# Kernel tuning notes

Hardware: AMD Instinct MI355X
Metric: run time of the kernel (lower is better)

## Reference

```python
import jax, jax.numpy as jnp
import numpy as np

B, N, F = 4, 1024, 128
HID, EMB = 64, 32  # node_transform hidden, node embedding dim


def setup_inputs() -> dict:
    key = jax.random.key(0)
    ks = jax.random.split(key, 12)
    s = lambda fan_in: 1.0 / np.sqrt(fan_in)
    x = jax.random.normal(ks[0], (B, N, F), dtype=jnp.float32)
    adj_matrix = jax.random.uniform(ks[1], (N, N), dtype=jnp.float32)
    # node_transform: Linear(F, 64) -> ReLU -> Linear(64, 32)
    W1 = jax.random.uniform(ks[2], (F, HID), minval=-s(F), maxval=s(F))
    b1 = jax.random.uniform(ks[3], (HID,), minval=-s(F), maxval=s(F))
    W2 = jax.random.uniform(ks[4], (HID, EMB), minval=-s(HID), maxval=s(HID))
    b2 = jax.random.uniform(ks[5], (EMB,), minval=-s(HID), maxval=s(HID))
    # edge_attention: Linear(64, 32) -> ReLU -> Linear(32, 1) -> Sigmoid
    Wa1 = jax.random.uniform(ks[6], (2 * EMB, 32), minval=-s(2 * EMB), maxval=s(2 * EMB))
    ba1 = jax.random.uniform(ks[7], (32,), minval=-s(2 * EMB), maxval=s(2 * EMB))
    Wa2 = jax.random.uniform(ks[8], (32, 1), minval=-s(32), maxval=s(32))
    ba2 = jax.random.uniform(ks[9], (1,), minval=-s(32), maxval=s(32))
    return {"x": x, "adj_matrix": adj_matrix, "W1": W1, "b1": b1, "W2": W2,
            "b2": b2, "Wa1": Wa1, "ba1": ba1, "Wa2": Wa2, "ba2": ba2}


def reference(x, adj_matrix, W1, b1, W2, b2, Wa1, ba1, Wa2, ba2):
    # node_transform: [B,N,F] -> [B,N,32]
    h = jax.nn.relu(x @ W1 + b1)
    e = h @ W2 + b2  # node embeddings [B,N,EMB]
    # edge attention on concat(e_i, e_j): the first Linear on the concat
    # decomposes exactly as e_i @ Wa1[:EMB] + e_j @ Wa1[EMB:] + ba1,
    # avoiding the [B,N,N,2*EMB] concat tensor.
    a_i = e @ Wa1[:EMB]   # [B,N,32]
    a_j = e @ Wa1[EMB:]   # [B,N,32]
    pre = jax.nn.relu(a_i[:, :, None, :] + a_j[:, None, :, :] + ba1)  # [B,N,N,32]
    att = jax.nn.sigmoid(jnp.squeeze(pre @ Wa2, -1) + ba2[0])  # [B,N,N]
    att = att * adj_matrix[None, :, :]
    attended = jnp.einsum('bij,bjd->bid', att, e)  # [B,N,EMB]
    return jnp.mean(attended, axis=1)  # [B,EMB]
```

## Files before the change

kernel.cpp:

```cpp
#include <hip/hip_runtime.h>

#define B   4
#define N   1024
#define F   128
#define HID 64
#define EMB 32
#define NIC 32
#define IC  (N/NIC)
#define JB  256

__global__ __launch_bounds__(256) void k1_embed(
    const float* __restrict__ x,  const float* __restrict__ W1, const float* __restrict__ b1,
    const float* __restrict__ W2, const float* __restrict__ b2,
    const float* __restrict__ Wa1,
    float* __restrict__ e, float* __restrict__ ai, float* __restrict__ aj)
{
    __shared__ float sh_x[4][F];
    __shared__ float sh_h[4][HID];
    __shared__ float sh_e[4][EMB];
    const int tid  = threadIdx.x;
    const int w    = tid >> 6;
    const int lane = tid & 63;
    const int r    = blockIdx.x * 4 + w;

    sh_x[w][lane]      = x[(size_t)r * F + lane];
    sh_x[w][lane + 64] = x[(size_t)r * F + 64 + lane];
    __syncthreads();

    float acc = b1[lane];
    #pragma unroll 8
    for (int k = 0; k < F; ++k)
        acc = fmaf(sh_x[w][k], W1[k * HID + lane], acc);
    sh_h[w][lane] = fmaxf(acc, 0.f);
    __syncthreads();

    const int d = lane & 31;
    float ev = b2[d];
    #pragma unroll 8
    for (int k = 0; k < HID; ++k)
        ev = fmaf(sh_h[w][k], W2[k * EMB + d], ev);
    if (lane < EMB) {
        sh_e[w][d] = ev;
        e[(size_t)r * EMB + d] = ev;
    }
    __syncthreads();

    const float* Wp = Wa1 + (lane < 32 ? 0 : EMB * EMB);
    float av = 0.f;
    #pragma unroll 8
    for (int k = 0; k < EMB; ++k)
        av = fmaf(sh_e[w][k], Wp[k * EMB + d], av);
    if (lane < 32) ai[(size_t)r * EMB + d] = av;
    else           aj[(size_t)r * EMB + d] = av;
}

__global__ __launch_bounds__(256) void k2_att(
    const float* __restrict__ ai, const float* __restrict__ aj,
    const float* __restrict__ ba1, const float* __restrict__ Wa2,
    const float* __restrict__ ba2, const float* __restrict__ adj,
    float* __restrict__ s_part)
{
    const int ic   = blockIdx.x;
    const int b    = blockIdx.y >> 2;
    const int jblk = blockIdx.y & 3;
    const int tid  = threadIdx.x;
    const int j    = jblk * JB + tid;

    __shared__ float4 sh_ai[IC][EMB / 4];
    {
        const int row = tid >> 3, c4 = tid & 7;
        const float4* src = (const float4*)(ai + ((size_t)b * N + ic * IC + row) * EMB);
        sh_ai[row][c4] = src[c4];
    }

    float ajb[EMB];
    {
        const float* ap = aj + ((size_t)b * N + j) * EMB;
        #pragma unroll
        for (int d2 = 0; d2 < EMB; ++d2) ajb[d2] = ap[d2] + ba1[d2];
    }
    float w2r[EMB];
    #pragma unroll
    for (int d2 = 0; d2 < EMB; ++d2) w2r[d2] = Wa2[d2];
    const float bb = ba2[0];
    __syncthreads();

    float ssum = 0.f;
    const float* adjp = adj + (size_t)(ic * IC) * N + j;
    for (int i = 0; i < IC; ++i) {
        const float4* arow = sh_ai[i];
        float dot = bb;
        #pragma unroll
        for (int q = 0; q < EMB / 4; ++q) {
            const float4 a4 = arow[q];
            dot = fmaf(fmaxf(a4.x + ajb[4 * q + 0], 0.f), w2r[4 * q + 0], dot);
            dot = fmaf(fmaxf(a4.y + ajb[4 * q + 1], 0.f), w2r[4 * q + 1], dot);
            dot = fmaf(fmaxf(a4.z + ajb[4 * q + 2], 0.f), w2r[4 * q + 2], dot);
            dot = fmaf(fmaxf(a4.w + ajb[4 * q + 3], 0.f), w2r[4 * q + 3], dot);
        }
        const float sg = 1.f / (1.f + __expf(-dot));
        ssum = fmaf(sg, adjp[(size_t)i * N], ssum);
    }
    s_part[((size_t)b * NIC + ic) * N + j] = ssum;
}

__global__ __launch_bounds__(256) void k3_out(
    const float* __restrict__ s_part, const float* __restrict__ e,
    float* __restrict__ out)
{
    const int b   = blockIdx.x;
    const int tid = threadIdx.x;
    float acc[EMB];
    #pragma unroll
    for (int d = 0; d < EMB; ++d) acc[d] = 0.f;

    for (int j = tid; j < N; j += 256) {
        float ssum = 0.f;
        #pragma unroll 8
        for (int ic = 0; ic < NIC; ++ic)
            ssum += s_part[((size_t)b * NIC + ic) * N + j];
        const float* ep = e + ((size_t)b * N + j) * EMB;
        #pragma unroll
        for (int d = 0; d < EMB; ++d) acc[d] = fmaf(ssum, ep[d], acc[d]);
    }

    __shared__ float red[256][EMB + 1];
    #pragma unroll
    for (int d = 0; d < EMB; ++d) red[tid][d] = acc[d];
    __syncthreads();
    if (tid < EMB) {
        float s = 0.f;
        for (int t = 0; t < 256; ++t) s += red[t][tid];
        out[b * EMB + tid] = s * (1.0f / N);
    }
}

extern "C" void kernel_launch(void* const* d_in, const int* in_sizes, int n_in,
                              void* d_out, int out_size, void* d_ws, size_t ws_size,
                              hipStream_t stream) {
    const float* x    = (const float*)d_in[0];
    const float* adj  = (const float*)d_in[1];
    const float* W1   = (const float*)d_in[2];
    const float* b1   = (const float*)d_in[3];
    const float* W2   = (const float*)d_in[4];
    const float* b2   = (const float*)d_in[5];
    const float* Wa1  = (const float*)d_in[6];
    const float* ba1  = (const float*)d_in[7];
    const float* Wa2  = (const float*)d_in[8];
    const float* ba2  = (const float*)d_in[9];
    float* out = (float*)d_out;

    float* ws = (float*)d_ws;
    float* e      = ws;
    float* ai     = ws + 131072;
    float* aj     = ws + 262144;
    float* s_part = ws + 393216;

    k1_embed<<<(B * N) / 4, 256, 0, stream>>>(x, W1, b1, W2, b2, Wa1, e, ai, aj);
    k2_att<<<dim3(NIC, B * (N / JB)), 256, 0, stream>>>(ai, aj, ba1, Wa2, ba2, adj, s_part);
    k3_out<<<B, 256, 0, stream>>>(s_part, e, out);
}
```

Before: 42.23 us.

## Fuse attention-weighted embedding reduction into attention kernel and increase i-chunk parallelism

The attention kernel now multiplies its per-column attention sums by the embeddings in-block and writes small per-block EMB-sized partials, so the final kernel only sums partials instead of re-reading s_part and e with just 4 blocks. The number of row chunks grows from 32 to 128 (8 rows each), giving 2048 blocks in place of 512. Adjacency values are prefetched into registers, the dot product uses four independent accumulators, and the sigmoid uses a fast reciprocal. Risks include extra per-block reduction overhead and a slightly different floating-point summation order.

Result: slower. 45.65 us (+8.1%).

```diff
diff --git a/kernel.cpp b/kernel.cpp
--- a/kernel.cpp
+++ b/kernel.cpp
@@ -5,9 +5,10 @@
 #define F   128
 #define HID 64
 #define EMB 32
-#define NIC 32
+#define NIC 128
 #define IC  (N/NIC)
 #define JB  256
+#define NCH (NIC*4)
 
 __global__ __launch_bounds__(256) void k1_embed(
     const float* __restrict__ x,  const float* __restrict__ W1, const float* __restrict__ b1,
@@ -28,7 +29,7 @@
     __syncthreads();
 
     float acc = b1[lane];
-    #pragma unroll 8
+    #pragma unroll 16
     for (int k = 0; k < F; ++k)
         acc = fmaf(sh_x[w][k], W1[k * HID + lane], acc);
     sh_h[w][lane] = fmaxf(acc, 0.f);
@@ -36,7 +37,7 @@
 
     const int d = lane & 31;
     float ev = b2[d];
-    #pragma unroll 8
+    #pragma unroll 16
     for (int k = 0; k < HID; ++k)
         ev = fmaf(sh_h[w][k], W2[k * EMB + d], ev);
     if (lane < EMB) {
@@ -47,7 +48,7 @@
 
     const float* Wp = Wa1 + (lane < 32 ? 0 : EMB * EMB);
     float av = 0.f;
-    #pragma unroll 8
+    #pragma unroll 16
     for (int k = 0; k < EMB; ++k)
         av = fmaf(sh_e[w][k], Wp[k * EMB + d], av);
     if (lane < 32) ai[(size_t)r * EMB + d] = av;
@@ -58,79 +59,104 @@
     const float* __restrict__ ai, const float* __restrict__ aj,
     const float* __restrict__ ba1, const float* __restrict__ Wa2,
     const float* __restrict__ ba2, const float* __restrict__ adj,
-    float* __restrict__ s_part)
+    const float* __restrict__ e, float* __restrict__ out_part)
 {
     const int ic   = blockIdx.x;
     const int b    = blockIdx.y >> 2;
     const int jblk = blockIdx.y & 3;
     const int tid  = threadIdx.x;
     const int j    = jblk * JB + tid;
+    const int i0   = ic * IC;
 
     __shared__ float4 sh_ai[IC][EMB / 4];
-    {
+    if (tid < IC * (EMB / 4)) {
         const int row = tid >> 3, c4 = tid & 7;
-        const float4* src = (const float4*)(ai + ((size_t)b * N + ic * IC + row) * EMB);
-        sh_ai[row][c4] = src[c4];
+        sh_ai[row][c4] =
+            ((const float4*)(ai + ((size_t)b * N + i0 + row) * EMB))[c4];
     }
 
     float ajb[EMB];
     {
-        const float* ap = aj + ((size_t)b * N + j) * EMB;
+        const float4* ap = (const float4*)(aj + ((size_t)b * N + j) * EMB);
+        const float4* bp = (const float4*)ba1;
         #pragma unroll
-        for (int d2 = 0; d2 < EMB; ++d2) ajb[d2] = ap[d2] + ba1[d2];
+        for (int q = 0; q < EMB / 4; ++q) {
+            const float4 a4 = ap[q], b4 = bp[q];
+            ajb[4 * q + 0] = a4.x + b4.x;
+            ajb[4 * q + 1] = a4.y + b4.y;
+            ajb[4 * q + 2] = a4.z + b4.z;
+            ajb[4 * q + 3] = a4.w + b4.w;
+        }
     }
-    float w2r[EMB];
+    float w2[EMB];
     #pragma unroll
-    for (int d2 = 0; d2 < EMB; ++d2) w2r[d2] = Wa2[d2];
+    for (int d2 = 0; d2 < EMB; ++d2) w2[d2] = Wa2[d2];
     const float bb = ba2[0];
+
+    float adjv[IC];
+    {
+        const float* adjp = adj + (size_t)i0 * N + j;
+        #pragma unroll
+        for (int i = 0; i < IC; ++i) adjv[i] = adjp[(size_t)i * N];
+    }
     __syncthreads();
 
     float ssum = 0.f;
-    const float* adjp = adj + (size_t)(ic * IC) * N + j;
+    #pragma unroll
     for (int i = 0; i < IC; ++i) {
         const float4* arow = sh_ai[i];
-        float dot = bb;
+        float acc0 = bb, acc1 = 0.f, acc2 = 0.f, acc3 = 0.f;
         #pragma unroll
         for (int q = 0; q < EMB / 4; ++q) {
             const float4 a4 = arow[q];
-            dot = fmaf(fmaxf(a4.x + ajb[4 * q + 0], 0.f), w2r[4 * q + 0], dot);
-            dot = fmaf(fmaxf(a4.y + ajb[4 * q + 1], 0.f), w2r[4 * q + 1], dot);
-            dot = fmaf(fmaxf(a4.z + ajb[4 * q + 2], 0.f), w2r[4 * q + 2], dot);
-            dot = fmaf(fmaxf(a4.w + ajb[4 * q + 3], 0.f), w2r[4 * q + 3], dot);
+            acc0 = fmaf(fmaxf(a4.x + ajb[4 * q + 0], 0.f), w2[4 * q + 0], acc0);
+            acc1 = fmaf(fmaxf(a4.y + ajb[4 * q + 1], 0.f), w2[4 * q + 1], acc1);
+            acc2 = fmaf(fmaxf(a4.z + ajb[4 * q + 2], 0.f), w2[4 * q + 2], acc2);
+            acc3 = fmaf(fmaxf(a4.w + ajb[4 * q + 3], 0.f), w2[4 * q + 3], acc3);
         }
-        const float sg = 1.f / (1.f + __expf(-dot));
-        ssum = fmaf(sg, adjp[(size_t)i * N], ssum);
+        const float dot = (acc0 + acc1) + (acc2 + acc3);
+        const float sg  = __builtin_amdgcn_rcpf(1.f + __expf(-dot));
+        ssum = fmaf(sg, adjv[i], ssum);
     }
-    s_part[((size_t)b * NIC + ic) * N + j] = ssum;
+
+    __shared__ float sh_s[JB];
+    sh_s[tid] = ssum;
+    __syncthreads();
+
+    const int d = tid & 31, g = tid >> 5;
+    const float* ep = e + ((size_t)b * N + jblk * JB + g * 32) * EMB + d;
+    float pacc = 0.f;
+    #pragma unroll
+    for (int jj = 0; jj < 32; ++jj)
+        pacc = fmaf(sh_s[g * 32 + jj], ep[(size_t)jj * EMB], pacc);
+
+    __shared__ float sh_r[8][EMB];
+    sh_r[g][d] = pacc;
+    __syncthreads();
+    if (tid < EMB) {
+        float s = 0.f;
+        #pragma unroll
+        for (int t = 0; t < 8; ++t) s += sh_r[t][tid];
+        out_part[((size_t)b * NCH + ic * 4 + jblk) * EMB + tid] = s;
+    }
 }
 
 __global__ __launch_bounds__(256) void k3_out(
-    const float* __restrict__ s_part, const float* __restrict__ e,
-    float* __restrict__ out)
+    const float* __restrict__ out_part, float* __restrict__ out)
 {
     const int b   = blockIdx.x;
     const int tid = threadIdx.x;
-    float acc[EMB];
-    #pragma unroll
-    for (int d = 0; d < EMB; ++d) acc[d] = 0.f;
-
-    for (int j = tid; j < N; j += 256) {
-        float ssum = 0.f;
-        #pragma unroll 8
-        for (int ic = 0; ic < NIC; ++ic)
-            ssum += s_part[((size_t)b * NIC + ic) * N + j];
-        const float* ep = e + ((size_t)b * N + j) * EMB;
-        #pragma unroll
-        for (int d = 0; d < EMB; ++d) acc[d] = fmaf(ssum, ep[d], acc[d]);
-    }
-
-    __shared__ float red[256][EMB + 1];
-    #pragma unroll
-    for (int d = 0; d < EMB; ++d) red[tid][d] = acc[d];
+    const int d = tid & 31, g = tid >> 5;
+    float acc = 0.f;
+    for (int c = g; c < NCH; c += 8)
+        acc += out_part[((size_t)b * NCH + c) * EMB + d];
+    __shared__ float sh[8][EMB];
+    sh[g][d] = acc;
     __syncthreads();
     if (tid < EMB) {
         float s = 0.f;
-        for (int t = 0; t < 256; ++t) s += red[t][tid];
+        #pragma unroll
+        for (int t = 0; t < 8; ++t) s += sh[t][tid];
         out[b * EMB + tid] = s * (1.0f / N);
     }
 }
@@ -151,12 +177,12 @@
     float* out = (float*)d_out;
 
     float* ws = (float*)d_ws;
-    float* e      = ws;
-    float* ai     = ws + 131072;
-    float* aj     = ws + 262144;
-    float* s_part = ws + 393216;
+    float* e        = ws;
+    float* ai       = ws + 131072;
+    float* aj       = ws + 262144;
+    float* out_part = ws + 393216;
 
     k1_embed<<<(B * N) / 4, 256, 0, stream>>>(x, W1, b1, W2, b2, Wa1, e, ai, aj);
-    k2_att<<<dim3(NIC, B * (N / JB)), 256, 0, stream>>>(ai, aj, ba1, Wa2, ba2, adj, s_part);
-    k3_out<<<B, 256, 0, stream>>>(s_part, e, out);
+    k2_att<<<dim3(NIC, B * 4), 256, 0, stream>>>(ai, aj, ba1, Wa2, ba2, adj, e, out_part);
+    k3_out<<<B, 256, 0, stream>>>(out_part, out);
 }
```
